# Kernel tuning notes

Measured on AMD Instinct MI355X. Metric: run time of the kernel, lower is better.

## Reference

```python
import jax, jax.numpy as jnp
import numpy as np

ALPHA = 0.2  # LeakyReLU negative slope
N, F_IN, F_OUT = 8192, 512, 64
NEG_INF = -9e15


def setup_inputs() -> dict:
    key = jax.random.key(0)
    k1, k2, k3, k4 = jax.random.split(key, 4)
    inp = jax.random.normal(k1, (N, F_IN), dtype=jnp.float32)
    adj = jax.random.randint(k2, (N, N), 0, 2, dtype=jnp.int32)
    W = jax.random.normal(k3, (F_IN, F_OUT), dtype=jnp.float32) * (1.414 / np.sqrt(F_IN))
    a = jax.random.normal(k4, (2 * F_OUT, 1), dtype=jnp.float32) * 0.1
    return {"input": inp, "adj": adj, "W": W, "a": a, "sparse": 0}


def reference(input, adj, W, a, sparse):
    h = input @ W  # [N, F_out]
    # Decompose concat([h_i, h_j]) @ a into additive src/dst terms (same math,
    # avoids the O(N^2 * 2F) intermediate): e_ij = leakyrelu(h_i@a1 + h_j@a2)
    f_src = h @ a[:F_OUT]   # [N, 1]
    f_dst = h @ a[F_OUT:]   # [N, 1]
    e = jax.nn.leaky_relu(f_src + f_dst.T, ALPHA)  # [N, N]
    attention = jnp.where(adj > 0, e, NEG_INF)
    attention = jax.nn.softmax(attention, axis=1)
    h_prime = attention @ h  # [N, F_out]
    return jax.nn.leaky_relu(h_prime, 0.01)[None]  # concat=True path; default F.leaky_relu slope 0.01
```

## Files before the change

kernel.cpp:

```cpp
#include <hip/hip_runtime.h>
#include <hip/hip_bf16.h>

#define N 8192
#define FIN 512
#define FOUT 64
#define ALPHA 0.2f

typedef __bf16 bf16x8 __attribute__((ext_vector_type(8)));
typedef __bf16 bf16x4 __attribute__((ext_vector_type(4)));
typedef float f32x4 __attribute__((ext_vector_type(4)));
typedef int i32x4 __attribute__((ext_vector_type(4)));


__device__ __forceinline__ unsigned enc_f(float x) {
    unsigned u = __float_as_uint(x);
    return (u & 0x80000000u) ? ~u : (u | 0x80000000u);
}
__device__ __forceinline__ float dec_f(unsigned u) {
    return (u & 0x80000000u) ? __uint_as_float(u & 0x7FFFFFFFu) : __uint_as_float(~u);
}

__global__ __launch_bounds__(64) void k_wt(const float* __restrict__ W,
                                           __bf16* __restrict__ WtG) {
    const int g = blockIdx.x * 64 + threadIdx.x;
    const int k = g >> 3;
    const int f0 = (g & 7) * 8;
    const float4 w0 = *(const float4*)(W + (size_t)k * FOUT + f0);
    const float4 w1 = *(const float4*)(W + (size_t)k * FOUT + f0 + 4);
    WtG[(size_t)(f0 + 0) * FIN + k] = (__bf16)w0.x;
    WtG[(size_t)(f0 + 1) * FIN + k] = (__bf16)w0.y;
    WtG[(size_t)(f0 + 2) * FIN + k] = (__bf16)w0.z;
    WtG[(size_t)(f0 + 3) * FIN + k] = (__bf16)w0.w;
    WtG[(size_t)(f0 + 4) * FIN + k] = (__bf16)w1.x;
    WtG[(size_t)(f0 + 5) * FIN + k] = (__bf16)w1.y;
    WtG[(size_t)(f0 + 6) * FIN + k] = (__bf16)w1.z;
    WtG[(size_t)(f0 + 7) * FIN + k] = (__bf16)w1.w;
}

__global__ __launch_bounds__(64) void k12(const float* __restrict__ in,
                                          const __bf16* __restrict__ WtG,
                                          const float* __restrict__ a,
                                          float* __restrict__ f_src,
                                          float* __restrict__ f_dst,
                                          unsigned* __restrict__ Mkey,
                                          __bf16* __restrict__ hT) {
    __shared__ __bf16 tb[64][16];
    const int lane = threadIdx.x;
    const int m = lane & 15, quad = lane >> 4;
    const int i0 = blockIdx.x * 16;

    f32x4 acc[4];
#pragma unroll
    for (int t = 0; t < 4; ++t) acc[t] = (f32x4){0.f, 0.f, 0.f, 0.f};

    const float* arow = in + (size_t)(i0 + m) * FIN + quad * 8;
    for (int k0 = 0; k0 < FIN; k0 += 32) {
        const float4 x0 = *(const float4*)(arow + k0);
        const float4 x1 = *(const float4*)(arow + k0 + 4);
        bf16x8 af;
        af[0] = (__bf16)x0.x; af[1] = (__bf16)x0.y; af[2] = (__bf16)x0.z; af[3] = (__bf16)x0.w;
        af[4] = (__bf16)x1.x; af[5] = (__bf16)x1.y; af[6] = (__bf16)x1.z; af[7] = (__bf16)x1.w;
#pragma unroll
        for (int t = 0; t < 4; ++t) {
            const bf16x8 bf = *(const bf16x8*)(WtG + (size_t)(t * 16 + m) * FIN + k0 + quad * 8);
            acc[t] = __builtin_amdgcn_mfma_f32_16x16x32_bf16(af, bf, acc[t], 0, 0, 0);
        }
    }
    float s1[4], s2[4];
#pragma unroll
    for (int r = 0; r < 4; ++r) { s1[r] = 0.f; s2[r] = 0.f; }
#pragma unroll
    for (int t = 0; t < 4; ++t) {
        const float a1 = a[t * 16 + m], a2 = a[64 + t * 16 + m];
#pragma unroll
        for (int r = 0; r < 4; ++r) {
            s1[r] += acc[t][r] * a1;
            s2[r] += acc[t][r] * a2;
        }
    }
#pragma unroll
    for (int off = 1; off <= 8; off <<= 1)
#pragma unroll
        for (int r = 0; r < 4; ++r) {
            s1[r] += __shfl_xor(s1[r], off);
            s2[r] += __shfl_xor(s2[r], off);
        }
    float lm = -1e30f;
    if (m == 0) {
#pragma unroll
        for (int r = 0; r < 4; ++r) {
            f_src[i0 + quad * 4 + r] = s1[r];
            f_dst[i0 + quad * 4 + r] = s2[r];
            lm = fmaxf(lm, s2[r]);
        }
    }
    lm = fmaxf(lm, __shfl_xor(lm, 16));
    lm = fmaxf(lm, __shfl_xor(lm, 32));
    if (lane == 0) atomicMax(Mkey, enc_f(lm));

#pragma unroll
    for (int t = 0; t < 4; ++t)
#pragma unroll
        for (int r = 0; r < 4; ++r) tb[t * 16 + m][quad * 4 + r] = (__bf16)acc[t][r];
    __syncthreads();
    {
        const int f = lane;
        const bf16x8 v0 = *(const bf16x8*)&tb[f][0];
        const bf16x8 v1 = *(const bf16x8*)&tb[f][8];
        *(bf16x8*)(hT + (size_t)f * N + i0) = v0;
        *(bf16x8*)(hT + (size_t)f * N + i0 + 8) = v1;
    }
}

constexpr int JT = 128;

__global__ __launch_bounds__(256, 4) void k3_attn(const int* __restrict__ adj,
                                                  const float* __restrict__ f_src,
                                                  const float* __restrict__ fdstG,
                                                  const unsigned* __restrict__ Mkey,
                                                  const __bf16* __restrict__ hT,
                                                  float* __restrict__ num_part,
                                                  float* __restrict__ lsum_part) {
    __shared__ __bf16 sh[64][JT + 8];
    __shared__ __bf16 wl[4][16][JT];
    __shared__ float sfd[1024];
    const int tid = threadIdx.x;
    const int wv = tid >> 6, lane = tid & 63;
    const int m = lane & 15, quad = lane >> 4;
    const int rpar = lane >> 5;
    const int col4 = (lane & 31) * 4;
    const int i0 = blockIdx.x * 64 + wv * 16;
    const int jb = blockIdx.y * 1024;
    const float LOG2E = 1.44269504088896f;

    *(f32x4*)&sfd[tid * 4] = *(const f32x4*)(fdstG + jb + tid * 4);

    const float M = dec_f(*Mkey);
    float fsr[16], shl[16];
#pragma unroll
    for (int r = 0; r < 16; ++r) {
        const float fs = f_src[i0 + r];
        const float t0 = fs + M;
        fsr[r] = fs;
        shl[r] = fmaxf(t0, ALPHA * t0) * LOG2E;
    }

    f32x4 acc[4];
#pragma unroll
    for (int t = 0; t < 4; ++t) acc[t] = (f32x4){0.f, 0.f, 0.f, 0.f};
    f32x4 accl = (f32x4){0.f, 0.f, 0.f, 0.f};

    bf16x8 bones;
#pragma unroll
    for (int jj = 0; jj < 8; ++jj) bones[jj] = (__bf16)(m == 0 ? 1.0f : 0.0f);

    const int* apL = adj + (size_t)(i0 + rpar) * N + jb + col4;

    for (int jt = 0; jt < 1024; jt += JT) {
        __syncthreads();

        i32x4 adjv[8];
#pragma unroll
        for (int v = 0; v < 8; ++v)
            adjv[v] = __builtin_nontemporal_load((const i32x4*)(apL + (size_t)(2 * v) * N + jt));

#pragma unroll
        for (int it = 0; it < 4; ++it) {
            const int c = tid + it * 256;
            const int f = c >> 4, off = (c & 15) * 8;
            *(bf16x8*)&sh[f][off] = *(const bf16x8*)(hT + (size_t)f * N + jb + jt + off);
        }
        __syncthreads();

        const f32x4 fd = *(const f32x4*)&sfd[jt + col4];
#pragma unroll
        for (int v = 0; v < 8; ++v) {
            const float fs_l = rpar ? fsr[2 * v + 1] : fsr[2 * v];
            const float sh_l = rpar ? shl[2 * v + 1] : shl[2 * v];
            const int rr = 2 * v + rpar;
            bf16x4 wb;
#pragma unroll
            for (int c = 0; c < 4; ++c) {
                float e = fs_l + fd[c];
                e = fmaxf(e, ALPHA * e);
                const float ex = __builtin_amdgcn_exp2f(e * LOG2E - sh_l);
                wb[c] = (__bf16)(adjv[v][c] > 0 ? ex : 0.f);
            }
            *(bf16x4*)&wl[wv][rr][col4 ^ ((rr & 7) << 3)] = wb;
        }

#pragma unroll
        for (int jj0 = 0; jj0 < JT; jj0 += 64) {
#pragma unroll
            for (int u = 0; u < 2; ++u) {
                const int cb = jj0 + u * 32 + quad * 8;
                const bf16x8 af = *(const bf16x8*)&wl[wv][m][cb ^ ((m & 7) << 3)];
#pragma unroll
                for (int t = 0; t < 4; ++t) {
                    const bf16x8 bfr = *(const bf16x8*)&sh[t * 16 + m][cb];
                    acc[t] = __builtin_amdgcn_mfma_f32_16x16x32_bf16(af, bfr, acc[t], 0, 0, 0);
                }
                accl = __builtin_amdgcn_mfma_f32_16x16x32_bf16(af, bones, accl, 0, 0, 0);
            }
        }
    }
    float* npb = num_part + (size_t)blockIdx.y * N * FOUT;
#pragma unroll
    for (int t = 0; t < 4; ++t)
#pragma unroll
        for (int r = 0; r < 4; ++r)
            npb[(size_t)(i0 + quad * 4 + r) * FOUT + t * 16 + m] = acc[t][r];
    if (m == 0) {
#pragma unroll
        for (int r = 0; r < 4; ++r)
            lsum_part[(size_t)blockIdx.y * N + i0 + quad * 4 + r] = accl[r];
    }
}

__global__ __launch_bounds__(256) void k4_norm(float* __restrict__ out,
                                               const float* __restrict__ num_part,
                                               const float* __restrict__ lsum_part) {
    const int idx = blockIdx.x * 256 + threadIdx.x;
    const int i = idx >> 6;
    float s = 0.f, l = 0.f;
#pragma unroll
    for (int p = 0; p < 8; ++p) {
        s += num_part[(size_t)p * N * FOUT + idx];
        l += lsum_part[(size_t)p * N + i];
    }
    const float v = s / (l > 0.f ? l : 1.f);
    out[idx] = v > 0.f ? v : 0.01f * v;
}

extern "C" void kernel_launch(void* const* d_in, const int* in_sizes, int n_in,
                              void* d_out, int out_size, void* d_ws, size_t ws_size,
                              hipStream_t stream) {
    const float* in = (const float*)d_in[0];
    const int* adj = (const int*)d_in[1];
    const float* W = (const float*)d_in[2];
    const float* a = (const float*)d_in[3];
    float* out = (float*)d_out;

    char* ws = (char*)d_ws;
    unsigned* Mkey = (unsigned*)ws;
    float* f_src = (float*)(ws + 32832);
    float* f_dst = (float*)(ws + 65600);
    __bf16* WtG = (__bf16*)(ws + 98368);
    __bf16* hT = (__bf16*)(ws + 163904);
    float* num_part = (float*)(ws + 1212480);
    float* lsum_part = (float*)(ws + 17989696);

    hipMemsetAsync(ws, 0, 64, stream);

    k_wt<<<64, 64, 0, stream>>>(W, WtG);
    k12<<<N / 16, 64, 0, stream>>>(in, WtG, a, f_src, f_dst, Mkey, hT);

    dim3 g3(N / 64, 8);
    k3_attn<<<g3, 256, 0, stream>>>(adj, f_src, f_dst, Mkey, hT, num_part, lsum_part);
    k4_norm<<<(N * FOUT) / 256, 256, 0, stream>>>(out, num_part, lsum_part);
}
```

Measured before the change: 394.8 us.

## Double-buffer attention tile loads with direct global-to-LDS prefetch

Restructures the attention kernel's j-tile loop into a software pipeline. The hT tile goes into a double-buffered, XOR-swizzled LDS array via global_load_lds, and the next tile's adjacency values are prefetched into registers while the current tile is computed. Sync uses manual waitcnt/s_barrier with scheduling fences, and f_src loads are made wave-uniform. This should hide global-load latency behind exp and MFMA work, at the cost of more registers and LDS, so occupancy hint drops from 4 to 3 blocks per CU.

```diff
diff --git a/kernel.cpp b/kernel.cpp
--- a/kernel.cpp
+++ b/kernel.cpp
@@ -19,6 +19,12 @@
 __device__ __forceinline__ float dec_f(unsigned u) {
     return (u & 0x80000000u) ? __uint_as_float(u & 0x7FFFFFFFu) : __uint_as_float(~u);
 }
+
+__device__ __forceinline__ void glds16(const void* g, void* l) {
+    __builtin_amdgcn_global_load_lds((const __attribute__((address_space(1))) void*)g,
+                                     (__attribute__((address_space(3))) void*)l, 16, 0, 0);
+}
+#define SFENCE() __builtin_amdgcn_sched_barrier(0)
 
 __global__ __launch_bounds__(64) void k_wt(const float* __restrict__ W,
                                            __bf16* __restrict__ WtG) {
@@ -114,14 +120,14 @@
 
 constexpr int JT = 128;
 
-__global__ __launch_bounds__(256, 4) void k3_attn(const int* __restrict__ adj,
+__global__ __launch_bounds__(256, 3) void k3_attn(const int* __restrict__ adj,
                                                   const float* __restrict__ f_src,
                                                   const float* __restrict__ fdstG,
                                                   const unsigned* __restrict__ Mkey,
                                                   const __bf16* __restrict__ hT,
                                                   float* __restrict__ num_part,
                                                   float* __restrict__ lsum_part) {
-    __shared__ __bf16 sh[64][JT + 8];
+    __shared__ __bf16 sh[2][64][JT];
     __shared__ __bf16 wl[4][16][JT];
     __shared__ float sfd[1024];
     const int tid = threadIdx.x;
@@ -134,74 +140,105 @@
     const float LOG2E = 1.44269504088896f;
 
     *(f32x4*)&sfd[tid * 4] = *(const f32x4*)(fdstG + jb + tid * 4);
-
     const float M = dec_f(*Mkey);
     float fsr[16], shl[16];
 #pragma unroll
     for (int r = 0; r < 16; ++r) {
-        const float fs = f_src[i0 + r];
+        const float fs =
+            __uint_as_float(__builtin_amdgcn_readfirstlane(__float_as_uint(f_src[i0 + r])));
         const float t0 = fs + M;
         fsr[r] = fs;
         shl[r] = fmaxf(t0, ALPHA * t0) * LOG2E;
     }
+    const __bf16* gsrc[4];
+#pragma unroll
+    for (int i = 0; i < 4; ++i) {
+        const int f = (wv * 4 + i) * 4 + (lane >> 4);
+        const int csw = ((lane & 15) * 8) ^ ((f & 7) << 3);
+        gsrc[i] = hT + (size_t)f * N + jb + csw;
+    }
+    const int* apL = adj + (size_t)(i0 + rpar) * N + jb + col4;
+
+    SFENCE();
+    __syncthreads();
+    SFENCE();
 
     f32x4 acc[4];
 #pragma unroll
     for (int t = 0; t < 4; ++t) acc[t] = (f32x4){0.f, 0.f, 0.f, 0.f};
     f32x4 accl = (f32x4){0.f, 0.f, 0.f, 0.f};
-
     bf16x8 bones;
 #pragma unroll
     for (int jj = 0; jj < 8; ++jj) bones[jj] = (__bf16)(m == 0 ? 1.0f : 0.0f);
 
-    const int* apL = adj + (size_t)(i0 + rpar) * N + jb + col4;
-
-    for (int jt = 0; jt < 1024; jt += JT) {
-        __syncthreads();
-
-        i32x4 adjv[8];
-#pragma unroll
-        for (int v = 0; v < 8; ++v)
-            adjv[v] = __builtin_nontemporal_load((const i32x4*)(apL + (size_t)(2 * v) * N + jt));
-
-#pragma unroll
-        for (int it = 0; it < 4; ++it) {
-            const int c = tid + it * 256;
-            const int f = c >> 4, off = (c & 15) * 8;
-            *(bf16x8*)&sh[f][off] = *(const bf16x8*)(hT + (size_t)f * N + jb + jt + off);
-        }
-        __syncthreads();
-
-        const f32x4 fd = *(const f32x4*)&sfd[jt + col4];
+    i32x4 adjv[2][8];
+#pragma unroll
+    for (int i = 0; i < 4; ++i) glds16(gsrc[i], &sh[0][(wv * 4 + i) * 4][0]);
+    SFENCE();
+#pragma unroll
+    for (int v = 0; v < 8; ++v)
+        adjv[0][v] = __builtin_nontemporal_load((const i32x4*)(apL + (size_t)(2 * v) * N));
+    SFENCE();
+
+#pragma unroll
+    for (int t = 0; t < 8; ++t) {
+        const int jt = t * JT;
+        const int cur = t & 1, nxt = cur ^ 1;
+        asm volatile("s_waitcnt vmcnt(8)" ::: "memory");
+        SFENCE();
+        __builtin_amdgcn_s_barrier();
+        SFENCE();
+        if (t < 7) {
+#pragma unroll
+            for (int i = 0; i < 4; ++i)
+                glds16(gsrc[i] + jt + JT, &sh[nxt][(wv * 4 + i) * 4][0]);
+        }
+        SFENCE();
+        if (t < 7) {
+#pragma unroll
+            for (int v = 0; v < 8; ++v)
+                adjv[nxt][v] = __builtin_nontemporal_load(
+                    (const i32x4*)(apL + (size_t)(2 * v) * N + jt + JT));
+        }
+        SFENCE();
+        const f32x4 fd0 = *(const f32x4*)&sfd[jt + col4];
 #pragma unroll
         for (int v = 0; v < 8; ++v) {
             const float fs_l = rpar ? fsr[2 * v + 1] : fsr[2 * v];
             const float sh_l = rpar ? shl[2 * v + 1] : shl[2 * v];
-            const int rr = 2 * v + rpar;
             bf16x4 wb;
 #pragma unroll
             for (int c = 0; c < 4; ++c) {
-                float e = fs_l + fd[c];
+                float e = fs_l + fd0[c];
                 e = fmaxf(e, ALPHA * e);
                 const float ex = __builtin_amdgcn_exp2f(e * LOG2E - sh_l);
-                wb[c] = (__bf16)(adjv[v][c] > 0 ? ex : 0.f);
+                wb[c] = (__bf16)(adjv[cur][v][c] > 0 ? ex : 0.f);
             }
+            const int rr = 2 * v + rpar;
             *(bf16x4*)&wl[wv][rr][col4 ^ ((rr & 7) << 3)] = wb;
         }
-
+        SFENCE();
 #pragma unroll
         for (int jj0 = 0; jj0 < JT; jj0 += 64) {
 #pragma unroll
             for (int u = 0; u < 2; ++u) {
                 const int cb = jj0 + u * 32 + quad * 8;
-                const bf16x8 af = *(const bf16x8*)&wl[wv][m][cb ^ ((m & 7) << 3)];
-#pragma unroll
-                for (int t = 0; t < 4; ++t) {
-                    const bf16x8 bfr = *(const bf16x8*)&sh[t * 16 + m][cb];
-                    acc[t] = __builtin_amdgcn_mfma_f32_16x16x32_bf16(af, bfr, acc[t], 0, 0, 0);
+                const int cs = cb ^ ((m & 7) << 3);
+                const bf16x8 af = *(const bf16x8*)&wl[wv][m][cs];
+#pragma unroll
+                for (int tt = 0; tt < 4; ++tt) {
+                    const bf16x8 bfr = *(const bf16x8*)&sh[cur][tt * 16 + m][cs];
+                    acc[tt] = __builtin_amdgcn_mfma_f32_16x16x32_bf16(af, bfr, acc[tt], 0, 0, 0);
                 }
                 accl = __builtin_amdgcn_mfma_f32_16x16x32_bf16(af, bones, accl, 0, 0, 0);
             }
+        }
+        SFENCE();
+        if (t < 7) {
+            asm volatile("s_waitcnt lgkmcnt(0)" ::: "memory");
+            SFENCE();
+            __builtin_amdgcn_s_barrier();
+            SFENCE();
         }
     }
     float* npb = num_part + (size_t)blockIdx.y * N * FOUT;
```

Measured after the change: 390.2 us. About the same (-1.2%).
